# Kernel tuning notes

Measured on AMD Instinct MI355X. Metric: run time of the kernel, lower is better.

## Reference

```python
import jax, jax.numpy as jnp
import numpy as np

B, DIN, DOUT = 16, 64, 64
P1_, P2_, P3_ = 64, 32, 16
BN_EPS = 1e-5


def setup_inputs() -> dict:
    key = jax.random.key(0)
    ks = jax.random.split(key, 8)
    A = jax.random.normal(ks[0], (B, DIN, P1_, P2_, P3_), dtype=jnp.float32)
    ini_p = float(np.sqrt(3.0 / DOUT / DIN))
    ini_qk = float(np.sqrt(1.0 / DOUT / DIN))
    def uni(k, s):
        return jax.random.uniform(k, (DOUT, DIN), dtype=jnp.float32, minval=-s, maxval=s)
    return {
        "A": A,
        "P1": uni(ks[1], ini_p),
        "P2": uni(ks[2], ini_p),
        "P3": uni(ks[3], ini_p),
        "P4": uni(ks[4], ini_p),
        "q": uni(ks[5], ini_qk),
        "k": uni(ks[6], ini_qk),
        "gamma": jnp.ones((DOUT,), jnp.float32),
        "beta": jnp.zeros((DOUT,), jnp.float32),
        "permutation_size1": P1_,
        "permutation_size2": P2_,
        "permutation_size3": P3_,
        "BATCH_SIZE": B,
    }


def reference(A, P1, P2, P3, P4, q, k, gamma, beta,
              permutation_size1, permutation_size2, permutation_size3, BATCH_SIZE):
    b = BATCH_SIZE
    dout = P1.shape[0]
    p1, p2, p3 = permutation_size1, permutation_size2, permutation_size3
    # branch 1: full per-element channel mix  [B, dout, p1, p2, p3]
    A1 = jnp.einsum('oi,bixyz->boxyz', P1, A)
    # branch 2: mean over p3, project, broadcast over p3
    A2 = jnp.einsum('oi,bixy->boxy', P2, A.mean(-1))[..., None]
    # branch 3: mean over p2, project, broadcast over p2
    A3 = jnp.einsum('oi,bixz->boxz', P3, A.mean(-2))[:, :, :, None, :]
    # attention over p1 with flattened (p2*p3) as the contraction axis
    Q = jnp.einsum('oi,bixyz->boxyz', q, A).reshape(b, dout, p1, p2 * p3)
    K = jnp.einsum('oi,bixyz->boxyz', k, A).reshape(b, dout, p1, p2 * p3)
    Alpha = jnp.einsum('bcxm,bcym->bcxy', Q, K)  # [B, dout, p1, p1]
    Alpha_norm = jnp.abs(Alpha) / jnp.linalg.norm(Alpha, axis=3, keepdims=True)
    V = jnp.einsum('oi,bixyz->boxyz', P4, A).reshape(b, dout, p1, p2 * p3)
    Y = jnp.einsum('bcxy,bcym->bcxm', Alpha_norm, V).reshape(b, dout, p1, p2, p3)
    out = A1 + 0.1 * A2 + 0.1 * A3 + 0.1 * Y
    out = jax.nn.relu(out)
    # BatchNorm3d (training-mode batch statistics, biased variance)
    mean = out.mean(axis=(0, 2, 3, 4), keepdims=True)
    var = out.var(axis=(0, 2, 3, 4), keepdims=True)
    out = (out - mean) * jax.lax.rsqrt(var + BN_EPS)
    out = out * gamma[None, :, None, None, None] + beta[None, :, None, None, None]
    return out
```

## Files before the change

kernel.cpp:

```cpp
#include <hip/hip_runtime.h>

typedef __attribute__((ext_vector_type(8))) short short8;
typedef __attribute__((ext_vector_type(4))) float f32x4;
typedef __attribute__((ext_vector_type(8))) unsigned short u16x8;
typedef __attribute__((ext_vector_type(4))) unsigned short u16x4;
typedef __attribute__((ext_vector_type(4))) unsigned int u32x4;
typedef unsigned short u16;

#define DEVINL __device__ __forceinline__

DEVINL u16 f2bf(float f) {
  unsigned u = __builtin_bit_cast(unsigned, f);
  unsigned r = (u + 0x7fffu + ((u >> 16) & 1u)) >> 16;
  return (u16)r;
}
DEVINL float bf2f(u16 h) {
  unsigned u = ((unsigned)h) << 16;
  return __builtin_bit_cast(float, u);
}
DEVINL unsigned pk2(float a, float b) {
  return (unsigned)f2bf(a) | ((unsigned)f2bf(b) << 16);
}
DEVINL int swzc(int row, int chunk) { return chunk ^ ((row ^ (row >> 3)) & 7); }
DEVINL int tile_byte(int row, int chunk) { return row * 128 + swzc(row, chunk) * 16; }

__global__ void kw_convert(const float* __restrict__ P1, const float* __restrict__ q,
                           const float* __restrict__ k, const float* __restrict__ P4,
                           const float* __restrict__ P2, const float* __restrict__ P3,
                           u16* __restrict__ Wbf) {
  int t = threadIdx.x;
  const float* srcs[6] = {P1, q, k, P4, P2, P3};
  for (int w = 0; w < 6; ++w)
    for (int e = t; e < 4096; e += 256) Wbf[w * 4096 + e] = f2bf(srcs[w][e]);
}

__global__ __launch_bounds__(512) void k_projA(
    const float* __restrict__ A, const u16* __restrict__ Wbf, u16* __restrict__ A1,
    u16* __restrict__ Q, u16* __restrict__ Km, u16* __restrict__ V,
    float* __restrict__ A2g, float* __restrict__ m2p, int g0) {
  __shared__ __align__(16) u16 tile[256 * 64];
  __shared__ __align__(16) u16 meanT[16 * 64];
  const int t = threadIdx.x;
  const int w = t >> 6, l = t & 63;
  const int lr = l & 15, lh = l >> 4;
  const int T = blockIdx.x, bg = blockIdx.y;
  const int x = T >> 1, h = T & 1;
  const long bglob = g0 + bg;

  const int m = w & 3, sh = w >> 2;
  const u16* wb = Wbf + m * 4096;
  short8 wf[4][2];
#pragma unroll
  for (int ot = 0; ot < 4; ++ot)
#pragma unroll
    for (int ks = 0; ks < 2; ++ks)
      wf[ot][ks] = *(const short8*)(wb + (ot * 16 + lr) * 64 + ks * 32 + lh * 8);
  u16* outp = (m == 0) ? A1 : (m == 1) ? Q : (m == 2) ? Km : V;
  outp += (long)bg * 64 * 32768;
  const int odd = lh & 1;
  const int p8 = (lh >> 1) * 8;

  {
    const int s4 = t & 31, i4 = t >> 5;
    const float* ap =
        A + (bglob * 64 + i4 * 4) * 32768 + (long)x * 512 + h * 256 + s4 * 4;
#pragma unroll
    for (int si = 0; si < 2; ++si) {
      f32x4 v0 = *(const f32x4*)(ap + si * 128);
      f32x4 v1 = *(const f32x4*)(ap + si * 128 + 32768);
      f32x4 v2 = *(const f32x4*)(ap + si * 128 + 65536);
      f32x4 v3 = *(const f32x4*)(ap + si * 128 + 98304);
#pragma unroll
      for (int e = 0; e < 4; ++e) {
        int s = si * 128 + s4 * 4 + e;
        u16x4 pk = {f2bf(v0[e]), f2bf(v1[e]), f2bf(v2[e]), f2bf(v3[e])};
        *(u16x4*)((char*)tile + tile_byte(s, i4 >> 1) + (i4 & 1) * 8) = pk;
      }
    }
  }
  __syncthreads();

  {
    const int ic = t & 7, zq = (t >> 3) & 3, y16 = t >> 5;
    float acc[8] = {0, 0, 0, 0, 0, 0, 0, 0};
#pragma unroll
    for (int zz = 0; zz < 4; ++zz) {
      int row = y16 * 16 + zq * 4 + zz;
      u16x8 v = *(const u16x8*)((const char*)tile + tile_byte(row, ic));
#pragma unroll
      for (int e = 0; e < 8; ++e) acc[e] += bf2f(v[e]);
    }
#pragma unroll
    for (int e = 0; e < 8; ++e) {
      acc[e] += __shfl_xor(acc[e], 8);
      acc[e] += __shfl_xor(acc[e], 16);
    }
    if (zq == 0) {
      u16x8 pk;
#pragma unroll
      for (int e = 0; e < 8; ++e) pk[e] = f2bf(acc[e] * (1.0f / 16.0f));
      *(u16x8*)((char*)meanT + tile_byte(y16, ic)) = pk;
    }
  }
  {
    const int ic = t & 7, yg = (t >> 3) & 3, z = t >> 5;
    float acc[8] = {0, 0, 0, 0, 0, 0, 0, 0};
#pragma unroll
    for (int yy = 0; yy < 4; ++yy) {
      int row = (yg * 4 + yy) * 16 + z;
      u16x8 v = *(const u16x8*)((const char*)tile + tile_byte(row, ic));
#pragma unroll
      for (int e = 0; e < 8; ++e) acc[e] += bf2f(v[e]);
    }
#pragma unroll
    for (int e = 0; e < 8; ++e) {
      acc[e] += __shfl_xor(acc[e], 8);
      acc[e] += __shfl_xor(acc[e], 16);
    }
    if (yg == 0) {
      float* mp = m2p + (((long)bg * 64 + x) * 2 + h) * 1024 + z * 64 + ic * 8;
      *(f32x4*)(mp) = (f32x4){acc[0], acc[1], acc[2], acc[3]};
      *(f32x4*)(mp + 4) = (f32x4){acc[4], acc[5], acc[6], acc[7]};
    }
  }

  for (int stp = 0; stp < 4; ++stp) {
    const int srowE = sh * 128 + stp * 32 + lr;
    const int srowO = srowE + 16;
    short8 aE0 = *(const short8*)((const char*)tile + tile_byte(srowE, lh));
    short8 aE1 = *(const short8*)((const char*)tile + tile_byte(srowE, 4 + lh));
    short8 aO0 = *(const short8*)((const char*)tile + tile_byte(srowO, lh));
    short8 aO1 = *(const short8*)((const char*)tile + tile_byte(srowO, 4 + lh));
    const int sbase = x * 512 + h * 256 + sh * 128 + stp * 32 + odd * 16 + p8;
#pragma unroll
    for (int ot = 0; ot < 4; ++ot) {
      f32x4 accE = {0.0f, 0.0f, 0.0f, 0.0f}, accO = {0.0f, 0.0f, 0.0f, 0.0f};
      accE = __builtin_amdgcn_mfma_f32_16x16x32_bf16(aE0, wf[ot][0], accE, 0, 0, 0);
      accE = __builtin_amdgcn_mfma_f32_16x16x32_bf16(aE1, wf[ot][1], accE, 0, 0, 0);
      accO = __builtin_amdgcn_mfma_f32_16x16x32_bf16(aO0, wf[ot][0], accO, 0, 0, 0);
      accO = __builtin_amdgcn_mfma_f32_16x16x32_bf16(aO1, wf[ot][1], accO, 0, 0, 0);
      unsigned pE0 = pk2(accE[0], accE[1]), pE1 = pk2(accE[2], accE[3]);
      unsigned pO0 = pk2(accO[0], accO[1]), pO1 = pk2(accO[2], accO[3]);
      unsigned rE0 = __shfl_xor((int)pE0, 16), rE1 = __shfl_xor((int)pE1, 16);
      unsigned rO0 = __shfl_xor((int)pO0, 16), rO1 = __shfl_xor((int)pO1, 16);
      u32x4 sv;
      if (odd) sv = (u32x4){rO0, rO1, pO0, pO1};
      else     sv = (u32x4){pE0, pE1, rE0, rE1};
      *(u32x4*)(outp + (long)(ot * 16 + lr) * 32768 + sbase) = sv;
    }
  }
  __syncthreads();

  if (w == 0) {
    const u16* wb2 = Wbf + 4 * 4096;
    f32x4 acc2[4];
#pragma unroll
    for (int ot = 0; ot < 4; ++ot) acc2[ot] = {0.0f, 0.0f, 0.0f, 0.0f};
#pragma unroll
    for (int ks = 0; ks < 2; ++ks) {
      short8 mf = *(const short8*)((const char*)meanT + tile_byte(lr, ks * 4 + lh));
#pragma unroll
      for (int ot = 0; ot < 4; ++ot) {
        short8 w2f = *(const short8*)(wb2 + (ot * 16 + lr) * 64 + ks * 32 + lh * 8);
        acc2[ot] = __builtin_amdgcn_mfma_f32_16x16x32_bf16(w2f, mf, acc2[ot], 0, 0, 0);
      }
    }
#pragma unroll
    for (int ot = 0; ot < 4; ++ot)
#pragma unroll
      for (int r = 0; r < 4; ++r) {
        int o = ot * 16 + lh * 4 + r;
        A2g[(((long)bg * 64 + o) * 64 + x) * 32 + h * 16 + lr] = acc2[ot][r];
      }
  }
}

__global__ __launch_bounds__(256) void k_a3fin(const float* __restrict__ m2p,
                                               const float* __restrict__ P3,
                                               float* __restrict__ A3g, int g0) {
  __shared__ float m2s[16 * 65];
  const int t = threadIdx.x;
  const int x = blockIdx.x, bg = blockIdx.y;
  const float* mp = m2p + ((long)bg * 64 + x) * 2048;
  {
    int e = t * 4;
    int z = e >> 6, i = e & 63;
    f32x4 v0 = *(const f32x4*)(mp + e);
    f32x4 v1 = *(const f32x4*)(mp + 1024 + e);
#pragma unroll
    for (int j = 0; j < 4; ++j) m2s[z * 65 + i + j] = (v0[j] + v1[j]) * (1.0f / 32.0f);
  }
  __syncthreads();
  const int z = t & 15, og = t >> 4;
#pragma unroll
  for (int oo = 0; oo < 4; ++oo) {
    int o = og * 4 + oo;
    float acc = 0.0f;
#pragma unroll 8
    for (int i = 0; i < 64; ++i) acc += P3[o * 64 + i] * m2s[z * 65 + i];
    A3g[(((long)bg * 64 + o) * 64 + x) * 16 + z] = acc;
  }
}

__global__ __launch_bounds__(256) void k_attn(const u16* __restrict__ Qg,
                                              const u16* __restrict__ Kg,
                                              const u16* __restrict__ Vg,
                                              const u16* __restrict__ A1g,
                                              const float* __restrict__ A2g,
                                              const float* __restrict__ A3g,
                                              u16* __restrict__ outbf,
                                              float* __restrict__ partials, int g0) {
  __shared__ __align__(16) u16 Vt[2][4096];
  __shared__ __align__(16) u16 An[4096];
  __shared__ float red[8];
  const int t = threadIdx.x, w = t >> 6, l = t & 63;
  const int lr = l & 15, lh = l >> 4;
  const int c = blockIdx.x, bg = blockIdx.y;
  const long bglob = g0 + bg;
  const long base = ((long)bg * 64 + c) * 32768;
  const u16* Qp = Qg + base;
  const u16* Kp = Kg + base;
  const u16* Vp = Vg + base;
  const u16* A1p = A1g + base;

  const int m4 = t & 15, y4 = t >> 4;

  u16x4 vr[4];
#pragma unroll
  for (int r = 0; r < 4; ++r)
    vr[r] = *(const u16x4*)(Vp + (y4 * 4 + r) * 512 + m4 * 4);

  f32x4 accA[4];
#pragma unroll
  for (int yt = 0; yt < 4; ++yt) accA[yt] = {0.0f, 0.0f, 0.0f, 0.0f};
  {
    const u16* Qrow = Qp + (16 * w + lr) * 512 + lh * 8;
    const u16* Krow = Kp + lr * 512 + lh * 8;
    for (int mc = 0; mc < 8; ++mc) {
      const int cb = mc * 64;
      short8 qf0 = *(const short8*)(Qrow + cb);
      short8 qf1 = *(const short8*)(Qrow + cb + 32);
#pragma unroll
      for (int yt = 0; yt < 4; ++yt) {
        short8 kf0 = *(const short8*)(Krow + yt * 16 * 512 + cb);
        short8 kf1 = *(const short8*)(Krow + yt * 16 * 512 + cb + 32);
        accA[yt] = __builtin_amdgcn_mfma_f32_16x16x32_bf16(qf0, kf0, accA[yt], 0, 0, 0);
        accA[yt] = __builtin_amdgcn_mfma_f32_16x16x32_bf16(qf1, kf1, accA[yt], 0, 0, 0);
      }
    }
  }

  float rsq[4];
#pragma unroll
  for (int r = 0; r < 4; ++r) {
    float s = 0.0f;
#pragma unroll
    for (int yt = 0; yt < 4; ++yt) s += accA[yt][r] * accA[yt][r];
#pragma unroll
    for (int msk = 1; msk < 16; msk <<= 1) s += __shfl_xor(s, msk);
    rsq[r] = rsqrtf(s);
  }
#pragma unroll
  for (int yt = 0; yt < 4; ++yt)
#pragma unroll
    for (int r = 0; r < 4; ++r) {
      int xr = 16 * w + 4 * lh + r;
      int y = yt * 16 + lr;
      *(u16*)((char*)An + xr * 128 + swzc(xr, y >> 3) * 16 + (y & 7) * 2) =
          f2bf(fabsf(accA[yt][r]) * rsq[r]);
    }

  float ls = 0.0f, lsq = 0.0f;
  const float* A2p = A2g + ((long)bg * 64 + c) * 2048;
  const float* A3p = A3g + ((long)bg * 64 + c) * 1024;
  u16* outp = outbf + (bglob * 64 + c) * 32768;
  const int x = 16 * w + lr;
  const f32x4 a3v = *(const f32x4*)(A3p + x * 16 + lh * 4);

  for (int mc = 0; mc < 8; ++mc) {
    u16* vbuf = Vt[mc & 1];
#pragma unroll
    for (int ci = 0; ci < 4; ++ci) {
      int mrow = m4 * 4 + ci;
      u16x4 pk = {vr[0][ci], vr[1][ci], vr[2][ci], vr[3][ci]};
      *(u16x4*)((char*)vbuf + tile_byte(mrow, y4 >> 1) + (y4 & 1) * 8) = pk;
    }
    asm volatile("s_waitcnt lgkmcnt(0)" ::: "memory");
    __builtin_amdgcn_s_barrier();
    __builtin_amdgcn_sched_barrier(0);
    if (mc < 7) {
      const int nc = (mc + 1) * 64;
#pragma unroll
      for (int r = 0; r < 4; ++r)
        vr[r] = *(const u16x4*)(Vp + (y4 * 4 + r) * 512 + nc + m4 * 4);
    }

    f32x4 accY[4];
#pragma unroll
    for (int mt = 0; mt < 4; ++mt) accY[mt] = {0.0f, 0.0f, 0.0f, 0.0f};
#pragma unroll
    for (int ks = 0; ks < 2; ++ks) {
      short8 anf = *(const short8*)((const char*)An + tile_byte(16 * w + lr, ks * 4 + lh));
#pragma unroll
      for (int mt = 0; mt < 4; ++mt) {
        short8 vf = *(const short8*)((const char*)vbuf + tile_byte(mt * 16 + lr, ks * 4 + lh));
        accY[mt] = __builtin_amdgcn_mfma_f32_16x16x32_bf16(vf, anf, accY[mt], 0, 0, 0);
      }
    }
#pragma unroll
    for (int mt = 0; mt < 4; ++mt) {
      float a2v = A2p[x * 32 + mc * 4 + mt];
      int mbase = mc * 64 + mt * 16 + lh * 4;
      u16x4 a1v = *(const u16x4*)(A1p + x * 512 + mbase);
      u16x4 o;
#pragma unroll
      for (int r = 0; r < 4; ++r) {
        float val = bf2f(a1v[r]) + 0.1f * (a2v + a3v[r] + accY[mt][r]);
        val = fmaxf(val, 0.0f);
        o[r] = f2bf(val);
        ls += val;
        lsq += val * val;
      }
      *(u16x4*)(outp + x * 512 + mbase) = o;
    }
  }

#pragma unroll
  for (int off = 32; off > 0; off >>= 1) {
    ls += __shfl_xor(ls, off);
    lsq += __shfl_xor(lsq, off);
  }
  if (l == 0) {
    red[w] = ls;
    red[4 + w] = lsq;
  }
  __syncthreads();
  if (t == 0) {
    partials[2 * (bglob * 64 + c) + 0] = red[0] + red[1] + red[2] + red[3];
    partials[2 * (bglob * 64 + c) + 1] = red[4] + red[5] + red[6] + red[7];
  }
}

__global__ void k_stats(const float* __restrict__ partials, const float* __restrict__ gamma,
                        const float* __restrict__ beta, float* __restrict__ sb) {
  int c = threadIdx.x;
  if (c >= 64) return;
  float S = 0.0f, SQ = 0.0f;
  for (int b = 0; b < 16; ++b) {
    S += partials[2 * (b * 64 + c) + 0];
    SQ += partials[2 * (b * 64 + c) + 1];
  }
  const float N = 524288.0f;
  float mean = S / N;
  float var = SQ / N - mean * mean;
  float rs = rsqrtf(var + 1e-5f);
  float scale = gamma[c] * rs;
  sb[c] = scale;
  sb[64 + c] = beta[c] - mean * scale;
}

__global__ void k_bn(const u16* __restrict__ outbf, float* __restrict__ out,
                     const float* __restrict__ sb) {
  long idx = ((long)blockIdx.x * 256 + threadIdx.x) * 8;
  int c = (int)((idx >> 15) & 63);
  float scale = sb[c], bias = sb[64 + c];
  u16x8 v = *(const u16x8*)(outbf + idx);
  f32x4 o0, o1;
#pragma unroll
  for (int r = 0; r < 4; ++r) {
    o0[r] = bf2f(v[r]) * scale + bias;
    o1[r] = bf2f(v[4 + r]) * scale + bias;
  }
  *(f32x4*)(out + idx) = o0;
  *(f32x4*)(out + idx + 4) = o1;
}

extern "C" void kernel_launch(void* const* d_in, const int* in_sizes, int n_in, void* d_out,
                              int out_size, void* d_ws, size_t ws_size, hipStream_t stream) {
  (void)in_sizes; (void)n_in; (void)out_size;
  const float* A = (const float*)d_in[0];
  const float* P1 = (const float*)d_in[1];
  const float* P2 = (const float*)d_in[2];
  const float* P3 = (const float*)d_in[3];
  const float* P4 = (const float*)d_in[4];
  const float* q = (const float*)d_in[5];
  const float* k = (const float*)d_in[6];
  const float* gamma = (const float*)d_in[7];
  const float* beta = (const float*)d_in[8];
  float* out = (float*)d_out;
  char* ws = (char*)d_ws;

  u16* Wbf = (u16*)ws;
  float* partials = (float*)(ws + 49152);
  float* sb = (float*)(ws + 57344);
  const size_t GR = 65536;
  const size_t OUTBF = (size_t)16 * 64 * 32768 * 2;
  u16* outbf = (u16*)(ws + GR);
  const size_t SZ_M = (size_t)64 * 32768 * 2;
  const size_t SZ_A2 = (size_t)64 * 64 * 32 * 4;
  const size_t SZ_A3 = (size_t)64 * 64 * 16 * 4;
  const size_t SZ_M2 = (size_t)64 * 2 * 16 * 64 * 4;
  const size_t perb = 4 * SZ_M + SZ_A2 + SZ_A3 + SZ_M2;
  const size_t base0 = GR + OUTBF;
  int G = 1;
  if (ws_size > base0 + perb) G = (int)((ws_size - base0) / perb);
  if (G > 16) G = 16;
  if (G < 1) G = 1;

  u16* A1 = (u16*)(ws + base0);
  u16* Qw = (u16*)(ws + base0 + (size_t)G * SZ_M);
  u16* Kw = (u16*)(ws + base0 + (size_t)G * SZ_M * 2);
  u16* Vw = (u16*)(ws + base0 + (size_t)G * SZ_M * 3);
  float* A2 = (float*)(ws + base0 + (size_t)G * SZ_M * 4);
  float* A3 = (float*)((char*)A2 + (size_t)G * SZ_A2);
  float* m2p = (float*)((char*)A3 + (size_t)G * SZ_A3);

  kw_convert<<<1, 256, 0, stream>>>(P1, q, k, P4, P2, P3, Wbf);
  for (int g0 = 0; g0 < 16; g0 += G) {
    int Gc = (16 - g0) < G ? (16 - g0) : G;
    k_projA<<<dim3(128, Gc), 512, 0, stream>>>(A, Wbf, A1, Qw, Kw, Vw, A2, m2p, g0);
    k_a3fin<<<dim3(64, Gc), 256, 0, stream>>>(m2p, P3, A3, g0);
    k_attn<<<dim3(64, Gc), 256, 0, stream>>>(Qw, Kw, Vw, A1, A2, A3, outbf, partials, g0);
  }
  k_stats<<<1, 64, 0, stream>>>(partials, gamma, beta, sb);
  k_bn<<<16384, 256, 0, stream>>>(outbf, out, sb);
}
```

Baseline: 288.0 us.

## Stage Q and K chunks through swizzled LDS with register prefetch in attention

Replaces direct per-wave global loads of Q and K fragments in the QK^T MFMA loop with cooperative coalesced loads into swizzled LDS tiles, prefetching the next 64-column chunk into registers while the current chunk is computed. This removes the redundant global reads where every wave re-read the full K tile and issued strided row loads. In exchange it adds two barriers per chunk and 16 KB more shared memory, which may lower occupancy.

```diff
diff --git a/kernel.cpp b/kernel.cpp
--- a/kernel.cpp
+++ b/kernel.cpp
@@ -210,6 +210,7 @@
                                               const float* __restrict__ A3g,
                                               u16* __restrict__ outbf,
                                               float* __restrict__ partials, int g0) {
+  __shared__ __align__(16) u16 Qc[4096], Kc[4096];
   __shared__ __align__(16) u16 Vt[2][4096];
   __shared__ __align__(16) u16 An[4096];
   __shared__ float red[8];
@@ -233,21 +234,50 @@
   f32x4 accA[4];
 #pragma unroll
   for (int yt = 0; yt < 4; ++yt) accA[yt] = {0.0f, 0.0f, 0.0f, 0.0f};
-  {
-    const u16* Qrow = Qp + (16 * w + lr) * 512 + lh * 8;
-    const u16* Krow = Kp + lr * 512 + lh * 8;
-    for (int mc = 0; mc < 8; ++mc) {
-      const int cb = mc * 64;
-      short8 qf0 = *(const short8*)(Qrow + cb);
-      short8 qf1 = *(const short8*)(Qrow + cb + 32);
+
+  const int srow = t >> 3, scc = t & 7;
+  u16x8 qpre[2], kpre[2];
+#pragma unroll
+  for (int it = 0; it < 2; ++it) {
+    int row = srow + it * 32;
+    int gch = scc ^ ((row ^ (row >> 3)) & 7);
+    qpre[it] = *(const u16x8*)(Qp + row * 512 + gch * 8);
+    kpre[it] = *(const u16x8*)(Kp + row * 512 + gch * 8);
+  }
+  for (int mc = 0; mc < 8; ++mc) {
+#pragma unroll
+    for (int it = 0; it < 2; ++it) {
+      int row = srow + it * 32;
+      *(u16x8*)((char*)Qc + row * 128 + scc * 16) = qpre[it];
+      *(u16x8*)((char*)Kc + row * 128 + scc * 16) = kpre[it];
+    }
+    asm volatile("s_waitcnt lgkmcnt(0)" ::: "memory");
+    __builtin_amdgcn_s_barrier();
+    __builtin_amdgcn_sched_barrier(0);
+    if (mc < 7) {
+      const int nc = (mc + 1) * 64;
+#pragma unroll
+      for (int it = 0; it < 2; ++it) {
+        int row = srow + it * 32;
+        int gch = scc ^ ((row ^ (row >> 3)) & 7);
+        qpre[it] = *(const u16x8*)(Qp + row * 512 + nc + gch * 8);
+        kpre[it] = *(const u16x8*)(Kp + row * 512 + nc + gch * 8);
+      }
+    }
+    short8 qf[2];
+#pragma unroll
+    for (int ks = 0; ks < 2; ++ks)
+      qf[ks] = *(const short8*)((const char*)Qc + tile_byte(16 * w + lr, ks * 4 + lh));
+#pragma unroll
+    for (int ks = 0; ks < 2; ++ks)
 #pragma unroll
       for (int yt = 0; yt < 4; ++yt) {
-        short8 kf0 = *(const short8*)(Krow + yt * 16 * 512 + cb);
-        short8 kf1 = *(const short8*)(Krow + yt * 16 * 512 + cb + 32);
-        accA[yt] = __builtin_amdgcn_mfma_f32_16x16x32_bf16(qf0, kf0, accA[yt], 0, 0, 0);
-        accA[yt] = __builtin_amdgcn_mfma_f32_16x16x32_bf16(qf1, kf1, accA[yt], 0, 0, 0);
-      }
-    }
+        short8 kf = *(const short8*)((const char*)Kc + tile_byte(yt * 16 + lr, ks * 4 + lh));
+        accA[yt] = __builtin_amdgcn_mfma_f32_16x16x32_bf16(qf[ks], kf, accA[yt], 0, 0, 0);
+      }
+    asm volatile("s_waitcnt lgkmcnt(0)" ::: "memory");
+    __builtin_amdgcn_s_barrier();
+    __builtin_amdgcn_sched_barrier(0);
   }
 
   float rsq[4];
```

New measurement: 279.0 us. -3.1%, faster.
